# Performance work log

Hardware: AMD Instinct MI355X
Metric: run time of the kernel (lower is better)

The kernel has to match this reference:

```python
import jax, jax.numpy as jnp
import numpy as np

N = 1_000_000
H = 64   # hidden_dim
E = 4    # edge_dim
S = 3    # state_dim


def _linear_params(key, fan_in, fan_out):
    kw, kb = jax.random.split(key)
    bound = 1.0 / np.sqrt(fan_in)
    W = jax.random.uniform(kw, (fan_in, fan_out), jnp.float32, -bound, bound)
    b = jax.random.uniform(kb, (fan_out,), jnp.float32, -bound, bound)
    return W, b


def setup_inputs() -> dict:
    key = jax.random.key(0)
    k_pc, k1, k2, k3, kmu, klam = jax.random.split(key, 6)
    W1, b1 = _linear_params(k1, 2, H)
    W2, b2 = _linear_params(k2, H, H)
    W3, b3 = _linear_params(k3, H, H)
    Wmu, bmu = _linear_params(kmu, H, E)
    Wlam, blam = _linear_params(klam, H, S)
    point_cloud = jax.random.normal(k_pc, (N, 2), jnp.float32)
    return {
        "point_cloud": point_cloud,
        "W1": W1, "b1": b1,
        "W2": W2, "b2": b2,
        "W3": W3, "b3": b3,
        "Wmu": Wmu, "bmu": bmu,
        "Wlam": Wlam, "blam": blam,
    }


def reference(point_cloud, W1, b1, W2, b2, W3, b3, Wmu, bmu, Wlam, blam):
    # Fixed constraint matrix G (edge_dim x state_dim)
    G = jnp.array([[1.0, 0.0, 0.0],
                   [-1.0, 0.0, 0.0],
                   [0.0, 1.0, 0.0],
                   [0.0, -1.0, 0.0]], dtype=jnp.float32)

    # MLP encoder: (N,2) -> (N,H)
    h = jax.nn.relu(point_cloud @ W1 + b1)
    h = jax.nn.relu(h @ W2 + b2)
    h = jax.nn.relu(h @ W3 + b3)

    mu = (h @ Wmu + bmu).T     # (E, N)
    lam = (h @ Wlam + blam).T  # (S, N)

    # Hard projection for mu: relu, then per-column clip of ||G^T mu||_2 to <= 1.
    # Vectorized replacement of the original per-column Python loop.
    mu = jax.nn.relu(mu)
    gtm = G.T @ mu                               # (S, N)
    norm = jnp.linalg.norm(gtm, axis=0)          # (N,)
    scale = jnp.where(norm > 1.0, 1.0 / (norm + 1e-8), 1.0)
    mu = mu * scale[None, :]

    # Hard projection for lam: always normalize each column to unit norm.
    lam = lam / (jnp.linalg.norm(lam, axis=0, keepdims=True) + 1e-8)
    return mu, lam
```

## Files before the change

### kernel.cpp

```cpp
#include <hip/hip_runtime.h>

typedef _Float16 h2 __attribute__((ext_vector_type(2)));
typedef _Float16 h8 __attribute__((ext_vector_type(8)));
typedef float    f4 __attribute__((ext_vector_type(4)));

#define PI(t,r) (8*((r)>>2) + ((r)&3) + 4*((t)&1) + 32*((t)>>1))

#define FSTRIDE 29

union Frag { h8 v; h2 q[4]; f4 f; };

__device__ __forceinline__ h2 relu2(h2 a) {
    const h2 z = {};
    return __builtin_elementwise_max(a, z);
}

__device__ __forceinline__ h2 pkrtz(float a, float b) {
    return __builtin_bit_cast(h2, __builtin_amdgcn_cvt_pkrtz(a, b));
}

__device__ __forceinline__ void packB(const f4 (&a)[4], Frag (&B)[2]) {
    #pragma unroll
    for (int c = 0; c < 2; ++c) {
        #pragma unroll
        for (int hh = 0; hh < 2; ++hh) {
            const int t = 2*c + hh;
            B[c].q[2*hh + 0] = relu2(pkrtz(a[t][0], a[t][1]));
            B[c].q[2*hh + 1] = relu2(pkrtz(a[t][2], a[t][3]));
        }
    }
}

__global__ __launch_bounds__(256, 3)
void pihp_mfma(const float* __restrict__ pc,
               const float* __restrict__ W1, const float* __restrict__ b1,
               const float* __restrict__ W2, const float* __restrict__ b2,
               const float* __restrict__ W3, const float* __restrict__ b3,
               const float* __restrict__ Wmu, const float* __restrict__ bmu,
               const float* __restrict__ Wlam, const float* __restrict__ blam,
               float* __restrict__ out, int N)
{
    __shared__ f4 wblob[64 * FSTRIDE];

    const int tid  = threadIdx.x;
    const int lane = tid & 63;
    const int g    = lane >> 4;
    const int m    = lane & 15;
    const int sec  = tid >> 6;

    f4* myw = &wblob[lane * FSTRIDE];
    if (sec == 0) {
        #pragma unroll
        for (int t = 0; t < 2; ++t)
            #pragma unroll
            for (int c = 0; c < 2; ++c) {
                Frag fr;
                #pragma unroll
                for (int ii = 0; ii < 8; ++ii)
                    fr.v[ii] = (_Float16)W2[(32*c + 8*g + ii)*64 + PI(t, m)];
                myw[2*t + c] = fr.f;
            }
        #pragma unroll
        for (int c = 0; c < 2; ++c) {
            Frag fr;
            #pragma unroll
            for (int ii = 0; ii < 8; ++ii) {
                const int k = 32*c + 8*g + ii;
                float v = 0.0f;
                if (m < 4)      v = Wmu[k*4 + m];
                else if (m < 7) v = Wlam[k*3 + (m - 4)];
                fr.v[ii] = (_Float16)v;
            }
            myw[16 + c] = fr.f;
        }
    } else if (sec == 1) {
        #pragma unroll
        for (int t = 2; t < 4; ++t)
            #pragma unroll
            for (int c = 0; c < 2; ++c) {
                Frag fr;
                #pragma unroll
                for (int ii = 0; ii < 8; ++ii)
                    fr.v[ii] = (_Float16)W2[(32*c + 8*g + ii)*64 + PI(t, m)];
                myw[2*t + c] = fr.f;
            }
        #pragma unroll
        for (int t = 0; t < 4; ++t) {
            f4 bb;
            #pragma unroll
            for (int i = 0; i < 4; ++i) bb[i] = b2[PI(t, 4*g + i)];
            myw[18 + t] = bb;
        }
    } else if (sec == 2) {
        #pragma unroll
        for (int t = 0; t < 2; ++t)
            #pragma unroll
            for (int c = 0; c < 2; ++c) {
                Frag fr;
                #pragma unroll
                for (int ii = 0; ii < 8; ++ii)
                    fr.v[ii] = (_Float16)W3[(32*c + 8*g + ii)*64 + PI(t, m)];
                myw[8 + 2*t + c] = fr.f;
            }
        #pragma unroll
        for (int t = 0; t < 4; ++t) {
            f4 bb;
            #pragma unroll
            for (int i = 0; i < 4; ++i) bb[i] = b3[PI(t, 4*g + i)];
            myw[22 + t] = bb;
        }
    } else {
        #pragma unroll
        for (int t = 2; t < 4; ++t)
            #pragma unroll
            for (int c = 0; c < 2; ++c) {
                Frag fr;
                #pragma unroll
                for (int ii = 0; ii < 8; ++ii)
                    fr.v[ii] = (_Float16)W3[(32*c + 8*g + ii)*64 + PI(t, m)];
                myw[8 + 2*t + c] = fr.f;
            }
        f4 bb;
        #pragma unroll
        for (int i = 0; i < 4; ++i) {
            const int rr = 4*g + i;
            bb[i] = (rr < 4) ? bmu[rr] : (rr < 7 ? blam[rr - 4] : 0.0f);
        }
        myw[26] = bb;
    }

    h2 w1x[2][4], w1y[2][4], w1b[2][4];
    #pragma unroll
    for (int c = 0; c < 2; ++c)
        #pragma unroll
        for (int p = 0; p < 4; ++p) {
            const int k = 32*c + 8*g + 2*p;
            w1x[c][p][0] = (_Float16)W1[k];      w1x[c][p][1] = (_Float16)W1[k+1];
            w1y[c][p][0] = (_Float16)W1[64+k];   w1y[c][p][1] = (_Float16)W1[64+k+1];
            w1b[c][p][0] = (_Float16)b1[k];      w1b[c][p][1] = (_Float16)b1[k+1];
        }

    __syncthreads();

    const int wid = blockIdx.x * (blockDim.x >> 6) + sec;
    const int nw  = gridDim.x * (blockDim.x >> 6);
    const int nslab = (N + 15) >> 4;
    int per = (nslab + nw - 1) / nw;
    per = (per + 1) & ~1;
    const int s0 = wid * per;
    if (s0 >= nslab) return;
    const int s1 = (s0 + per < nslab) ? (s0 + per) : nslab;

    float* const pl0 = out;
    float* const pl1 = out + (size_t)N;
    float* const pl2 = out + (size_t)2*N;
    float* const pl3 = out + (size_t)3*N;
    float* const pl4 = out + (size_t)4*N;
    float* const pl5 = out + (size_t)5*N;
    float* const pl6 = out + (size_t)6*N;

    const float2* __restrict__ pcv = reinterpret_cast<const float2*>(pc);
    const int Nm1 = N - 1;
    auto clampload = [&](int ss) -> float2 {
        int pt = ss*16 + m;
        pt = pt < Nm1 ? pt : Nm1;
        return pcv[pt];
    };
    auto frag = [&](int i) -> h8 { return __builtin_bit_cast(h8, myw[i]); };

    float2 Pc0 = clampload(s0);
    float2 Pc1 = clampload(s0 + 1);
    const bool isMu = (g == 0);

    #pragma unroll 1
    for (int ss = s0; ss < s1; ss += 2) {
        asm volatile("" ::: "memory");

        float2 Pn0 = clampload(ss + 2);
        float2 Pn1 = clampload(ss + 3);

        Frag B0[2], B1[2];
        {
            const h2 x0 = pkrtz(Pc0.x, Pc0.x), y0 = pkrtz(Pc0.y, Pc0.y);
            const h2 x1 = pkrtz(Pc1.x, Pc1.x), y1 = pkrtz(Pc1.y, Pc1.y);
            #pragma unroll
            for (int c = 0; c < 2; ++c)
                #pragma unroll
                for (int p = 0; p < 4; ++p) {
                    B0[c].q[p] = relu2(x0 * w1x[c][p] + y0 * w1y[c][p] + w1b[c][p]);
                    B1[c].q[p] = relu2(x1 * w1x[c][p] + y1 * w1y[c][p] + w1b[c][p]);
                }
        }

        f4 a0[4], a1[4];

        #pragma unroll
        for (int t = 0; t < 4; ++t) {
            const h8 A  = frag(2*t);
            const f4 bc = myw[18 + t];
            a0[t] = __builtin_amdgcn_mfma_f32_16x16x32_f16(A, B0[0].v, bc, 0, 0, 0);
            a1[t] = __builtin_amdgcn_mfma_f32_16x16x32_f16(A, B1[0].v, bc, 0, 0, 0);
        }
        #pragma unroll
        for (int t = 0; t < 4; ++t) {
            const h8 A = frag(2*t + 1);
            a0[t] = __builtin_amdgcn_mfma_f32_16x16x32_f16(A, B0[1].v, a0[t], 0, 0, 0);
            a1[t] = __builtin_amdgcn_mfma_f32_16x16x32_f16(A, B1[1].v, a1[t], 0, 0, 0);
        }
        packB(a0, B0);
        packB(a1, B1);

        #pragma unroll
        for (int t = 0; t < 4; ++t) {
            const h8 A  = frag(8 + 2*t);
            const f4 bc = myw[22 + t];
            a0[t] = __builtin_amdgcn_mfma_f32_16x16x32_f16(A, B0[0].v, bc, 0, 0, 0);
            a1[t] = __builtin_amdgcn_mfma_f32_16x16x32_f16(A, B1[0].v, bc, 0, 0, 0);
        }
        #pragma unroll
        for (int t = 0; t < 4; ++t) {
            const h8 A = frag(8 + 2*t + 1);
            a0[t] = __builtin_amdgcn_mfma_f32_16x16x32_f16(A, B0[1].v, a0[t], 0, 0, 0);
            a1[t] = __builtin_amdgcn_mfma_f32_16x16x32_f16(A, B1[1].v, a1[t], 0, 0, 0);
        }
        packB(a0, B0);
        packB(a1, B1);

        f4 h0, h1;
        {
            const h8 Ah0 = frag(16), Ah1 = frag(17);
            const f4 bch = myw[26];
            h0 = __builtin_amdgcn_mfma_f32_16x16x32_f16(Ah0, B0[0].v, bch, 0, 0, 0);
            h1 = __builtin_amdgcn_mfma_f32_16x16x32_f16(Ah0, B1[0].v, bch, 0, 0, 0);
            h0 = __builtin_amdgcn_mfma_f32_16x16x32_f16(Ah1, B0[1].v, h0, 0, 0, 0);
            h1 = __builtin_amdgcn_mfma_f32_16x16x32_f16(Ah1, B1[1].v, h1, 0, 0, 0);
        }

        #pragma unroll
        for (int u = 0; u < 2; ++u) {
            const f4 hv = (u == 0) ? h0 : h1;
            const int pt = (ss + u)*16 + m;
            const float r0 = isMu ? fmaxf(hv[0], 0.0f) : hv[0];
            const float r1 = isMu ? fmaxf(hv[1], 0.0f) : hv[1];
            const float r2 = isMu ? fmaxf(hv[2], 0.0f) : hv[2];
            const float r3 = isMu ? fmaxf(hv[3], 0.0f) : hv[3];
            const float t0 = isMu ? (r0 - r1) : r0;
            const float t1 = isMu ? (r2 - r3) : r1;
            const float t2 = isMu ? 0.0f      : r2;
            const float ssum = t0*t0 + t1*t1 + t2*t2;
            const float r  = rsqrtf(ssum + 1e-16f);
            const float sc = isMu ? fminf(r, 1.0f) : r;
            if (pt < N) {
                if (g == 0) {
                    pl0[pt] = r0 * sc;
                    pl1[pt] = r1 * sc;
                    pl2[pt] = r2 * sc;
                    pl3[pt] = r3 * sc;
                } else if (g == 1) {
                    pl4[pt] = r0 * sc;
                    pl5[pt] = r1 * sc;
                    pl6[pt] = r2 * sc;
                }
            }
        }

        Pc0 = Pn0;
        Pc1 = Pn1;
    }
}

extern "C" void kernel_launch(void* const* d_in, const int* in_sizes, int n_in,
                              void* d_out, int out_size, void* d_ws, size_t ws_size,
                              hipStream_t stream) {
    const float* pc   = (const float*)d_in[0];
    const float* W1   = (const float*)d_in[1];
    const float* b1   = (const float*)d_in[2];
    const float* W2   = (const float*)d_in[3];
    const float* b2   = (const float*)d_in[4];
    const float* W3   = (const float*)d_in[5];
    const float* b3   = (const float*)d_in[6];
    const float* Wmu  = (const float*)d_in[7];
    const float* bmu  = (const float*)d_in[8];
    const float* Wlam = (const float*)d_in[9];
    const float* blam = (const float*)d_in[10];
    float* out = (float*)d_out;

    const int N = in_sizes[0] / 2;
    pihp_mfma<<<768, 256, 0, stream>>>(pc, W1, b1, W2, b2, W3, b3,
                                       Wmu, bmu, Wlam, blam, out, N);
}
```

Before: 34.45 us.

## Hoist MFMA weight fragments into registers and lower occupancy target

Loads the layer-2/3/head weight fragments and bias accumulators from LDS into registers once before the slab loop, pinned with empty asm constraints, so the inner loop issues no LDS reads. Launch bounds drop from 3 to 2 waves-per-SIMD blocks and the grid shrinks from 768 to 512 blocks to make room for the extra registers. The per-point bounds check on stores is removed, which is only safe when N is a multiple of 16 (true for N=1e6) and otherwise writes out of bounds. The memory clobber at the loop top is also dropped.

After: 33.24 us (median of 2 runs). 1.04x faster.

```diff
diff --git a/kernel.cpp b/kernel.cpp
--- a/kernel.cpp
+++ b/kernel.cpp
@@ -31,7 +31,7 @@
     }
 }
 
-__global__ __launch_bounds__(256, 3)
+__global__ __launch_bounds__(256, 2)
 void pihp_mfma(const float* __restrict__ pc,
                const float* __restrict__ W1, const float* __restrict__ b1,
                const float* __restrict__ W2, const float* __restrict__ b2,
@@ -142,6 +142,37 @@
 
     __syncthreads();
 
+    h8 A2f[4][2], A3f[4][2], Ahf[2];
+    f4 bC2[4], bC3[4], bCh;
+    #pragma unroll
+    for (int t = 0; t < 4; ++t)
+        #pragma unroll
+        for (int c = 0; c < 2; ++c) {
+            A2f[t][c] = __builtin_bit_cast(h8, myw[2*t + c]);
+            A3f[t][c] = __builtin_bit_cast(h8, myw[8 + 2*t + c]);
+        }
+    #pragma unroll
+    for (int c = 0; c < 2; ++c) Ahf[c] = __builtin_bit_cast(h8, myw[16 + c]);
+    #pragma unroll
+    for (int t = 0; t < 4; ++t) { bC2[t] = myw[18 + t]; bC3[t] = myw[22 + t]; }
+    bCh = myw[26];
+
+    #pragma unroll
+    for (int t = 0; t < 4; ++t)
+        #pragma unroll
+        for (int c = 0; c < 2; ++c) {
+            asm volatile("" : "+v"(A2f[t][c]));
+            asm volatile("" : "+v"(A3f[t][c]));
+        }
+    #pragma unroll
+    for (int c = 0; c < 2; ++c) asm volatile("" : "+v"(Ahf[c]));
+    #pragma unroll
+    for (int t = 0; t < 4; ++t) {
+        asm volatile("" : "+v"(bC2[t]));
+        asm volatile("" : "+v"(bC3[t]));
+    }
+    asm volatile("" : "+v"(bCh));
+
     const int wid = blockIdx.x * (blockDim.x >> 6) + sec;
     const int nw  = gridDim.x * (blockDim.x >> 6);
     const int nslab = (N + 15) >> 4;
@@ -166,7 +197,6 @@
         pt = pt < Nm1 ? pt : Nm1;
         return pcv[pt];
     };
-    auto frag = [&](int i) -> h8 { return __builtin_bit_cast(h8, myw[i]); };
 
     float2 Pc0 = clampload(s0);
     float2 Pc1 = clampload(s0 + 1);
@@ -174,8 +204,6 @@
 
     #pragma unroll 1
     for (int ss = s0; ss < s1; ss += 2) {
-        asm volatile("" ::: "memory");
-
         float2 Pn0 = clampload(ss + 2);
         float2 Pn1 = clampload(ss + 3);
 
@@ -196,45 +224,35 @@
 
         #pragma unroll
         for (int t = 0; t < 4; ++t) {
-            const h8 A  = frag(2*t);
-            const f4 bc = myw[18 + t];
-            a0[t] = __builtin_amdgcn_mfma_f32_16x16x32_f16(A, B0[0].v, bc, 0, 0, 0);
-            a1[t] = __builtin_amdgcn_mfma_f32_16x16x32_f16(A, B1[0].v, bc, 0, 0, 0);
-        }
-        #pragma unroll
-        for (int t = 0; t < 4; ++t) {
-            const h8 A = frag(2*t + 1);
-            a0[t] = __builtin_amdgcn_mfma_f32_16x16x32_f16(A, B0[1].v, a0[t], 0, 0, 0);
-            a1[t] = __builtin_amdgcn_mfma_f32_16x16x32_f16(A, B1[1].v, a1[t], 0, 0, 0);
+            a0[t] = __builtin_amdgcn_mfma_f32_16x16x32_f16(A2f[t][0], B0[0].v, bC2[t], 0, 0, 0);
+            a1[t] = __builtin_amdgcn_mfma_f32_16x16x32_f16(A2f[t][0], B1[0].v, bC2[t], 0, 0, 0);
+        }
+        #pragma unroll
+        for (int t = 0; t < 4; ++t) {
+            a0[t] = __builtin_amdgcn_mfma_f32_16x16x32_f16(A2f[t][1], B0[1].v, a0[t], 0, 0, 0);
+            a1[t] = __builtin_amdgcn_mfma_f32_16x16x32_f16(A2f[t][1], B1[1].v, a1[t], 0, 0, 0);
         }
         packB(a0, B0);
         packB(a1, B1);
 
         #pragma unroll
         for (int t = 0; t < 4; ++t) {
-            const h8 A  = frag(8 + 2*t);
-            const f4 bc = myw[22 + t];
-            a0[t] = __builtin_amdgcn_mfma_f32_16x16x32_f16(A, B0[0].v, bc, 0, 0, 0);
-            a1[t] = __builtin_amdgcn_mfma_f32_16x16x32_f16(A, B1[0].v, bc, 0, 0, 0);
-        }
-        #pragma unroll
-        for (int t = 0; t < 4; ++t) {
-            const h8 A = frag(8 + 2*t + 1);
-            a0[t] = __builtin_amdgcn_mfma_f32_16x16x32_f16(A, B0[1].v, a0[t], 0, 0, 0);
-            a1[t] = __builtin_amdgcn_mfma_f32_16x16x32_f16(A, B1[1].v, a1[t], 0, 0, 0);
+            a0[t] = __builtin_amdgcn_mfma_f32_16x16x32_f16(A3f[t][0], B0[0].v, bC3[t], 0, 0, 0);
+            a1[t] = __builtin_amdgcn_mfma_f32_16x16x32_f16(A3f[t][0], B1[0].v, bC3[t], 0, 0, 0);
+        }
+        #pragma unroll
+        for (int t = 0; t < 4; ++t) {
+            a0[t] = __builtin_amdgcn_mfma_f32_16x16x32_f16(A3f[t][1], B0[1].v, a0[t], 0, 0, 0);
+            a1[t] = __builtin_amdgcn_mfma_f32_16x16x32_f16(A3f[t][1], B1[1].v, a1[t], 0, 0, 0);
         }
         packB(a0, B0);
         packB(a1, B1);
 
         f4 h0, h1;
-        {
-            const h8 Ah0 = frag(16), Ah1 = frag(17);
-            const f4 bch = myw[26];
-            h0 = __builtin_amdgcn_mfma_f32_16x16x32_f16(Ah0, B0[0].v, bch, 0, 0, 0);
-            h1 = __builtin_amdgcn_mfma_f32_16x16x32_f16(Ah0, B1[0].v, bch, 0, 0, 0);
-            h0 = __builtin_amdgcn_mfma_f32_16x16x32_f16(Ah1, B0[1].v, h0, 0, 0, 0);
-            h1 = __builtin_amdgcn_mfma_f32_16x16x32_f16(Ah1, B1[1].v, h1, 0, 0, 0);
-        }
+        h0 = __builtin_amdgcn_mfma_f32_16x16x32_f16(Ahf[0], B0[0].v, bCh, 0, 0, 0);
+        h1 = __builtin_amdgcn_mfma_f32_16x16x32_f16(Ahf[0], B1[0].v, bCh, 0, 0, 0);
+        h0 = __builtin_amdgcn_mfma_f32_16x16x32_f16(Ahf[1], B0[1].v, h0, 0, 0, 0);
+        h1 = __builtin_amdgcn_mfma_f32_16x16x32_f16(Ahf[1], B1[1].v, h1, 0, 0, 0);
 
         #pragma unroll
         for (int u = 0; u < 2; ++u) {
@@ -250,17 +268,15 @@
             const float ssum = t0*t0 + t1*t1 + t2*t2;
             const float r  = rsqrtf(ssum + 1e-16f);
             const float sc = isMu ? fminf(r, 1.0f) : r;
-            if (pt < N) {
-                if (g == 0) {
-                    pl0[pt] = r0 * sc;
-                    pl1[pt] = r1 * sc;
-                    pl2[pt] = r2 * sc;
-                    pl3[pt] = r3 * sc;
-                } else if (g == 1) {
-                    pl4[pt] = r0 * sc;
-                    pl5[pt] = r1 * sc;
-                    pl6[pt] = r2 * sc;
-                }
+            if (g == 0) {
+                pl0[pt] = r0 * sc;
+                pl1[pt] = r1 * sc;
+                pl2[pt] = r2 * sc;
+                pl3[pt] = r3 * sc;
+            } else if (g == 1) {
+                pl4[pt] = r0 * sc;
+                pl5[pt] = r1 * sc;
+                pl6[pt] = r2 * sc;
             }
         }
 
@@ -286,6 +302,6 @@
     float* out = (float*)d_out;
 
     const int N = in_sizes[0] / 2;
-    pihp_mfma<<<768, 256, 0, stream>>>(pc, W1, b1, W2, b2, W3, b3,
+    pihp_mfma<<<512, 256, 0, stream>>>(pc, W1, b1, W2, b2, W3, b3,
                                        Wmu, bmu, Wlam, blam, out, N);
 }
```
